# Kernel optimization log

Hardware: AMD Instinct MI355X
Metric: run time of the kernel (lower is better)

Reference implementation:

```python
import jax, jax.numpy as jnp
import numpy as np

DIM_Q = 64
SCALE = DIM_Q ** 0.5


def setup_inputs() -> dict:
    key = jax.random.key(0)
    kq, kk = jax.random.split(key)
    Q = jax.random.normal(kq, (4, 4096, 64), dtype=jnp.float32)
    K = jax.random.normal(kk, (4, 4096, 64), dtype=jnp.float32)
    return {"Q": Q, "K": K}


def _cdist(Q, K):
    # ||q-k||_2 via expansion: ||q||^2 + ||k||^2 - 2 q.k  (matches torch.cdist p=2)
    q2 = jnp.sum(Q * Q, axis=-1, keepdims=True)          # [B,N,1]
    k2 = jnp.sum(K * K, axis=-1)[:, None, :]             # [B,1,M]
    qk = jnp.einsum('bnd,bmd->bnm', Q, K)                # [B,N,M]
    d2 = jnp.maximum(q2 + k2 - 2.0 * qk, 0.0)
    return jnp.sqrt(d2)


def reference(Q, K):
    scores = -_cdist(Q, K) / SCALE                       # [B,N,M]
    return jax.nn.softmax(scores, axis=-1)
```

## Files before the change

kernel.cpp:

```cpp
#include <hip/hip_runtime.h>
#include <hip/hip_bf16.h>

#define BATCH 4
#define NQ 4096
#define NK 4096
#define DIM 64

typedef __attribute__((ext_vector_type(8))) short bf16x8;
typedef __attribute__((ext_vector_type(4))) float f32x4;

__device__ __forceinline__ unsigned short f2bf(float f) {
  union { float f; unsigned u; } v; v.f = f;
  return (unsigned short)((v.u + 0x7FFF + ((v.u >> 16) & 1)) >> 16);
}

template<int ROWS>
__device__ __forceinline__ void stage_tile(const float* __restrict__ g, char* lds,
                                           float* sq, int tid) {
  constexpr int NV = ROWS * 16;
  #pragma unroll
  for (int i = 0; i < NV / 256; ++i) {
    const int idx = i * 256 + tid;
    const float4 v = reinterpret_cast<const float4*>(g)[idx];
    const int f = idx * 4;
    const int row = f >> 6, col = f & 63;
    uint2 pk;
    pk.x = (unsigned)f2bf(v.x) | ((unsigned)f2bf(v.y) << 16);
    pk.y = (unsigned)f2bf(v.z) | ((unsigned)f2bf(v.w) << 16);
    const int byte = row * 128 + ((((col >> 3) ^ (row & 7)) << 4)) + ((col >> 2) & 1) * 8;
    *reinterpret_cast<uint2*>(lds + byte) = pk;
  }
  if (tid < ROWS) {
    const float4* rp = reinterpret_cast<const float4*>(g + tid * DIM);
    float s = 0.f;
    #pragma unroll
    for (int j = 0; j < 16; ++j) {
      const float4 v = rp[j];
      s += v.x * v.x + v.y * v.y + v.z * v.z + v.w * v.w;
    }
    sq[tid] = s;
  }
}

__device__ __forceinline__ bf16x8 frag_load(const char* lds, int row, int ks, int lane) {
  return *reinterpret_cast<const bf16x8*>(
      lds + row * 128 + (((ks * 4 + (lane >> 4)) ^ (row & 7)) << 4));
}

__global__ __launch_bounds__(256) void k_rowsum(
    const float* __restrict__ Qg, const float* __restrict__ Kg,
    float* __restrict__ partials) {
  __shared__ char Qlds[64 * 128];
  __shared__ char Klds[256 * 128];
  __shared__ float q2[64];
  __shared__ float k2[256];
  const int tid = threadIdx.x;
  const int cs = blockIdx.x;
  const int brow = blockIdx.y * 64;
  const int b = blockIdx.z;
  const float* Qb = Qg + ((size_t)b * NQ + brow) * DIM;
  const float* Kb = Kg + (size_t)b * NK * DIM;

  stage_tile<64>(Qb, Qlds, q2, tid);
  __syncthreads();

  const int lane = tid & 63, w = tid >> 6;
  const int arow = w * 16 + (lane & 15);
  const bf16x8 af0 = frag_load(Qlds, arow, 0, lane);
  const bf16x8 af1 = frag_load(Qlds, arow, 1, lane);
  float q2r[4];
  #pragma unroll
  for (int i = 0; i < 4; ++i) q2r[i] = q2[w * 16 + (lane >> 4) * 4 + i];

  float sums[4] = {0.f, 0.f, 0.f, 0.f};
  for (int t = 0; t < 4; ++t) {
    __syncthreads();
    stage_tile<256>(Kb + ((size_t)(cs * 4 + t)) * 256 * DIM, Klds, k2, tid);
    __syncthreads();
    #pragma unroll
    for (int c = 0; c < 16; ++c) {
      const int krow = c * 16 + (lane & 15);
      const bf16x8 bf0 = frag_load(Klds, krow, 0, lane);
      const bf16x8 bf1 = frag_load(Klds, krow, 1, lane);
      f32x4 acc = {0.f, 0.f, 0.f, 0.f};
      acc = __builtin_amdgcn_mfma_f32_16x16x32_bf16(af0, bf0, acc, 0, 0, 0);
      acc = __builtin_amdgcn_mfma_f32_16x16x32_bf16(af1, bf1, acc, 0, 0, 0);
      const float k2c = k2[krow];
      #pragma unroll
      for (int i = 0; i < 4; ++i) {
        const float d2 = fmaxf(q2r[i] + k2c - 2.f * acc[i], 0.f);
        sums[i] += __expf(-sqrtf(d2) * 0.125f);
      }
    }
  }
  #pragma unroll
  for (int m = 1; m < 16; m <<= 1) {
    #pragma unroll
    for (int i = 0; i < 4; ++i) sums[i] += __shfl_xor(sums[i], m, 64);
  }
  if ((lane & 15) == 0) {
    const int r = brow + w * 16 + (lane >> 4) * 4;
    #pragma unroll
    for (int i = 0; i < 4; ++i)
      partials[((size_t)cs * BATCH + b) * NQ + r + i] = sums[i];
  }
}

__global__ __launch_bounds__(256) void k_softmax(
    const float* __restrict__ Qg, const float* __restrict__ Kg,
    const float* __restrict__ partials, float* __restrict__ out) {
  __shared__ char Qlds[64 * 128];
  __shared__ char Klds[256 * 128];
  __shared__ float q2[64];
  __shared__ float k2[256];
  const int tid = threadIdx.x;
  const int bcol = blockIdx.x * 256;
  const int brow = blockIdx.y * 64;
  const int b = blockIdx.z;
  const float* Qb = Qg + ((size_t)b * NQ + brow) * DIM;
  const float* Kb = Kg + ((size_t)b * NK + bcol) * DIM;

  stage_tile<64>(Qb, Qlds, q2, tid);
  stage_tile<256>(Kb, Klds, k2, tid);
  __syncthreads();

  const int lane = tid & 63, w = tid >> 6;
  const int arow = w * 16 + (lane & 15);
  const bf16x8 af0 = frag_load(Qlds, arow, 0, lane);
  const bf16x8 af1 = frag_load(Qlds, arow, 1, lane);

  float q2r[4], inv[4];
  size_t rowbase[4];
  #pragma unroll
  for (int i = 0; i < 4; ++i) {
    const int r = w * 16 + (lane >> 4) * 4 + i;
    q2r[i] = q2[r];
    const int gr = brow + r;
    float s = 0.f;
    #pragma unroll
    for (int cs = 0; cs < 4; ++cs) s += partials[((size_t)cs * BATCH + b) * NQ + gr];
    inv[i] = 1.0f / s;
    rowbase[i] = ((size_t)b * NQ + gr) * NK + bcol;
  }

  #pragma unroll
  for (int c = 0; c < 16; ++c) {
    const int krow = c * 16 + (lane & 15);
    const bf16x8 bf0 = frag_load(Klds, krow, 0, lane);
    const bf16x8 bf1 = frag_load(Klds, krow, 1, lane);
    f32x4 acc = {0.f, 0.f, 0.f, 0.f};
    acc = __builtin_amdgcn_mfma_f32_16x16x32_bf16(af0, bf0, acc, 0, 0, 0);
    acc = __builtin_amdgcn_mfma_f32_16x16x32_bf16(af1, bf1, acc, 0, 0, 0);
    const float k2c = k2[krow];
    const int col = c * 16 + (lane & 15);
    #pragma unroll
    for (int i = 0; i < 4; ++i) {
      const float d2 = fmaxf(q2r[i] + k2c - 2.f * acc[i], 0.f);
      out[rowbase[i] + col] = __expf(-sqrtf(d2) * 0.125f) * inv[i];
    }
  }
}

extern "C" void kernel_launch(void* const* d_in, const int* in_sizes, int n_in,
                              void* d_out, int out_size, void* d_ws, size_t ws_size,
                              hipStream_t stream) {
  const float* Q = (const float*)d_in[0];
  const float* K = (const float*)d_in[1];
  float* out = (float*)d_out;
  float* partials = (float*)d_ws;

  k_rowsum<<<dim3(4, NQ / 64, BATCH), dim3(256), 0, stream>>>(Q, K, partials);
  k_softmax<<<dim3(NK / 256, NQ / 64, BATCH), dim3(256), 0, stream>>>(Q, K, partials, out);
}
```

Baseline: 382.0 us.

## Compute scores once, store fp16 intermediates, then normalize in a separate scaling pass

Replaces the two-pass scheme (row-sum pass then recompute-and-write pass) with a single score pass that writes unnormalized exp values and per-block partial row sums. A small kernel inverts the summed partials and a streaming kernel rescales into the output. The score pass swaps MFMA operands so each lane stores four contiguous columns with vector stores. The fp16 intermediate halves the extra traffic but adds rounding error and needs a large workspace, falling back to in-place fp32 otherwise.

```diff
diff --git a/kernel.cpp b/kernel.cpp
--- a/kernel.cpp
+++ b/kernel.cpp
@@ -1,5 +1,6 @@
 #include <hip/hip_runtime.h>
 #include <hip/hip_bf16.h>
+#include <hip/hip_fp16.h>
 
 #define BATCH 4
 #define NQ 4096
@@ -47,68 +48,10 @@
       lds + row * 128 + (((ks * 4 + (lane >> 4)) ^ (row & 7)) << 4));
 }
 
-__global__ __launch_bounds__(256) void k_rowsum(
+template<bool F16WS>
+__global__ __launch_bounds__(256) void k_score(
     const float* __restrict__ Qg, const float* __restrict__ Kg,
-    float* __restrict__ partials) {
-  __shared__ char Qlds[64 * 128];
-  __shared__ char Klds[256 * 128];
-  __shared__ float q2[64];
-  __shared__ float k2[256];
-  const int tid = threadIdx.x;
-  const int cs = blockIdx.x;
-  const int brow = blockIdx.y * 64;
-  const int b = blockIdx.z;
-  const float* Qb = Qg + ((size_t)b * NQ + brow) * DIM;
-  const float* Kb = Kg + (size_t)b * NK * DIM;
-
-  stage_tile<64>(Qb, Qlds, q2, tid);
-  __syncthreads();
-
-  const int lane = tid & 63, w = tid >> 6;
-  const int arow = w * 16 + (lane & 15);
-  const bf16x8 af0 = frag_load(Qlds, arow, 0, lane);
-  const bf16x8 af1 = frag_load(Qlds, arow, 1, lane);
-  float q2r[4];
-  #pragma unroll
-  for (int i = 0; i < 4; ++i) q2r[i] = q2[w * 16 + (lane >> 4) * 4 + i];
-
-  float sums[4] = {0.f, 0.f, 0.f, 0.f};
-  for (int t = 0; t < 4; ++t) {
-    __syncthreads();
-    stage_tile<256>(Kb + ((size_t)(cs * 4 + t)) * 256 * DIM, Klds, k2, tid);
-    __syncthreads();
-    #pragma unroll
-    for (int c = 0; c < 16; ++c) {
-      const int krow = c * 16 + (lane & 15);
-      const bf16x8 bf0 = frag_load(Klds, krow, 0, lane);
-      const bf16x8 bf1 = frag_load(Klds, krow, 1, lane);
-      f32x4 acc = {0.f, 0.f, 0.f, 0.f};
-      acc = __builtin_amdgcn_mfma_f32_16x16x32_bf16(af0, bf0, acc, 0, 0, 0);
-      acc = __builtin_amdgcn_mfma_f32_16x16x32_bf16(af1, bf1, acc, 0, 0, 0);
-      const float k2c = k2[krow];
-      #pragma unroll
-      for (int i = 0; i < 4; ++i) {
-        const float d2 = fmaxf(q2r[i] + k2c - 2.f * acc[i], 0.f);
-        sums[i] += __expf(-sqrtf(d2) * 0.125f);
-      }
-    }
-  }
-  #pragma unroll
-  for (int m = 1; m < 16; m <<= 1) {
-    #pragma unroll
-    for (int i = 0; i < 4; ++i) sums[i] += __shfl_xor(sums[i], m, 64);
-  }
-  if ((lane & 15) == 0) {
-    const int r = brow + w * 16 + (lane >> 4) * 4;
-    #pragma unroll
-    for (int i = 0; i < 4; ++i)
-      partials[((size_t)cs * BATCH + b) * NQ + r + i] = sums[i];
-  }
-}
-
-__global__ __launch_bounds__(256) void k_softmax(
-    const float* __restrict__ Qg, const float* __restrict__ Kg,
-    const float* __restrict__ partials, float* __restrict__ out) {
+    void* __restrict__ score, float* __restrict__ partials) {
   __shared__ char Qlds[64 * 128];
   __shared__ char Klds[256 * 128];
   __shared__ float q2[64];
@@ -125,39 +68,93 @@
   __syncthreads();
 
   const int lane = tid & 63, w = tid >> 6;
-  const int arow = w * 16 + (lane & 15);
-  const bf16x8 af0 = frag_load(Qlds, arow, 0, lane);
-  const bf16x8 af1 = frag_load(Qlds, arow, 1, lane);
+  const int qrow = w * 16 + (lane & 15);
+  const bf16x8 qf0 = frag_load(Qlds, qrow, 0, lane);
+  const bf16x8 qf1 = frag_load(Qlds, qrow, 1, lane);
+  const float q2r = q2[qrow];
+  const int g = lane >> 4;
 
-  float q2r[4], inv[4];
-  size_t rowbase[4];
-  #pragma unroll
-  for (int i = 0; i < 4; ++i) {
-    const int r = w * 16 + (lane >> 4) * 4 + i;
-    q2r[i] = q2[r];
-    const int gr = brow + r;
-    float s = 0.f;
-    #pragma unroll
-    for (int cs = 0; cs < 4; ++cs) s += partials[((size_t)cs * BATCH + b) * NQ + gr];
-    inv[i] = 1.0f / s;
-    rowbase[i] = ((size_t)b * NQ + gr) * NK + bcol;
-  }
+  float rowsum = 0.f;
+  const size_t rbase = ((size_t)b * NQ + brow + qrow) * NK + bcol + g * 4;
 
   #pragma unroll
   for (int c = 0; c < 16; ++c) {
     const int krow = c * 16 + (lane & 15);
-    const bf16x8 bf0 = frag_load(Klds, krow, 0, lane);
-    const bf16x8 bf1 = frag_load(Klds, krow, 1, lane);
+    const bf16x8 kf0 = frag_load(Klds, krow, 0, lane);
+    const bf16x8 kf1 = frag_load(Klds, krow, 1, lane);
     f32x4 acc = {0.f, 0.f, 0.f, 0.f};
-    acc = __builtin_amdgcn_mfma_f32_16x16x32_bf16(af0, bf0, acc, 0, 0, 0);
-    acc = __builtin_amdgcn_mfma_f32_16x16x32_bf16(af1, bf1, acc, 0, 0, 0);
-    const float k2c = k2[krow];
-    const int col = c * 16 + (lane & 15);
+    acc = __builtin_amdgcn_mfma_f32_16x16x32_bf16(kf0, qf0, acc, 0, 0, 0);
+    acc = __builtin_amdgcn_mfma_f32_16x16x32_bf16(kf1, qf1, acc, 0, 0, 0);
+    const float4 k2v = *reinterpret_cast<const float4*>(k2 + c * 16 + g * 4);
+
+    float e[4];
+    const float k2a[4] = {k2v.x, k2v.y, k2v.z, k2v.w};
     #pragma unroll
     for (int i = 0; i < 4; ++i) {
-      const float d2 = fmaxf(q2r[i] + k2c - 2.f * acc[i], 0.f);
-      out[rowbase[i] + col] = __expf(-sqrtf(d2) * 0.125f) * inv[i];
+      const float d2 = fmaxf(q2r + k2a[i] - 2.f * acc[i], 0.f);
+      e[i] = __expf(-0.125f * sqrtf(d2));
     }
+    if (F16WS) {
+      const __half h0 = __float2half_rn(e[0]), h1 = __float2half_rn(e[1]);
+      const __half h2 = __float2half_rn(e[2]), h3 = __float2half_rn(e[3]);
+      rowsum += __half2float(h0) + __half2float(h1) +
+                __half2float(h2) + __half2float(h3);
+      uint2 pk;
+      pk.x = (unsigned)__half_as_ushort(h0) | ((unsigned)__half_as_ushort(h1) << 16);
+      pk.y = (unsigned)__half_as_ushort(h2) | ((unsigned)__half_as_ushort(h3) << 16);
+      *reinterpret_cast<uint2*>((__half*)score + rbase + c * 16) = pk;
+    } else {
+      rowsum += e[0] + e[1] + e[2] + e[3];
+      float4 st = {e[0], e[1], e[2], e[3]};
+      *reinterpret_cast<float4*>((float*)score + rbase + c * 16) = st;
+    }
+  }
+
+  rowsum += __shfl_xor(rowsum, 16, 64);
+  rowsum += __shfl_xor(rowsum, 32, 64);
+  if (lane < 16)
+    partials[((size_t)blockIdx.x * BATCH + b) * NQ + brow + w * 16 + lane] = rowsum;
+}
+
+__global__ __launch_bounds__(256) void k_inv(
+    const float* __restrict__ partials, float* __restrict__ inv) {
+  const int idx = blockIdx.x * 256 + threadIdx.x;
+  float s = 0.f;
+  #pragma unroll
+  for (int p = 0; p < 16; ++p) s += partials[(size_t)p * (BATCH * NQ) + idx];
+  inv[idx] = 1.f / s;
+}
+
+__global__ __launch_bounds__(256) void k_scale_f16(
+    const __half* __restrict__ sc, const float* __restrict__ inv,
+    float* __restrict__ out) {
+  const size_t nchunk = (size_t)BATCH * NQ * NK / 8;
+  const size_t stride = (size_t)gridDim.x * blockDim.x;
+  for (size_t c = (size_t)blockIdx.x * blockDim.x + threadIdx.x; c < nchunk; c += stride) {
+    const int rg = (int)(c >> 9);
+    const float iv = inv[rg];
+    union { uint4 u; __half h[8]; } U;
+    U.u = reinterpret_cast<const uint4*>(sc)[c];
+    float4 a, bq;
+    a.x = __half2float(U.h[0]) * iv; a.y = __half2float(U.h[1]) * iv;
+    a.z = __half2float(U.h[2]) * iv; a.w = __half2float(U.h[3]) * iv;
+    bq.x = __half2float(U.h[4]) * iv; bq.y = __half2float(U.h[5]) * iv;
+    bq.z = __half2float(U.h[6]) * iv; bq.w = __half2float(U.h[7]) * iv;
+    float4* op = reinterpret_cast<float4*>(out) + 2 * c;
+    op[0] = a; op[1] = bq;
+  }
+}
+
+__global__ __launch_bounds__(256) void k_scale_f32(
+    const float* __restrict__ inv, float* __restrict__ out) {
+  const size_t nchunk = (size_t)BATCH * NQ * NK / 4;
+  const size_t stride = (size_t)gridDim.x * blockDim.x;
+  for (size_t c = (size_t)blockIdx.x * blockDim.x + threadIdx.x; c < nchunk; c += stride) {
+    const int rg = (int)(c >> 10);
+    const float iv = inv[rg];
+    float4 v = reinterpret_cast<float4*>(out)[c];
+    v.x *= iv; v.y *= iv; v.z *= iv; v.w *= iv;
+    reinterpret_cast<float4*>(out)[c] = v;
   }
 }
 
@@ -167,8 +164,23 @@
   const float* Q = (const float*)d_in[0];
   const float* K = (const float*)d_in[1];
   float* out = (float*)d_out;
+
+  const size_t P_BYTES = (size_t)16 * BATCH * NQ * 4;
+  const size_t I_BYTES = (size_t)BATCH * NQ * 4;
+  const size_t S_BYTES = (size_t)BATCH * NQ * NK * 2;
   float* partials = (float*)d_ws;
+  float* inv = (float*)((char*)d_ws + P_BYTES);
+  __half* sc = (__half*)((char*)d_ws + P_BYTES + I_BYTES);
 
-  k_rowsum<<<dim3(4, NQ / 64, BATCH), dim3(256), 0, stream>>>(Q, K, partials);
-  k_softmax<<<dim3(NK / 256, NQ / 64, BATCH), dim3(256), 0, stream>>>(Q, K, partials, out);
+  if (ws_size >= P_BYTES + I_BYTES + S_BYTES) {
+    k_score<true><<<dim3(NK / 256, NQ / 64, BATCH), dim3(256), 0, stream>>>(
+        Q, K, (void*)sc, partials);
+    k_inv<<<dim3(BATCH * NQ / 256), dim3(256), 0, stream>>>(partials, inv);
+    k_scale_f16<<<dim3(2048), dim3(256), 0, stream>>>(sc, inv, out);
+  } else {
+    k_score<false><<<dim3(NK / 256, NQ / 64, BATCH), dim3(256), 0, stream>>>(
+        Q, K, (void*)out, partials);
+    k_inv<<<dim3(BATCH * NQ / 256), dim3(256), 0, stream>>>(partials, inv);
+    k_scale_f32<<<dim3(2048), dim3(256), 0, stream>>>(inv, out);
+  }
 }
```

After: 400.2 us. 1.05x slower.

## Swap MFMA operands so each lane owns a row and stores float4 outputs

Applied to the files above, without the earlier changes.

The MFMA operand order is swapped (K fragment first, Q second), so each lane's four accumulator values fall in one query row across four consecutive key columns. This lets the write kernel emit one 16-byte vectorized store per tile instead of four scattered scalar stores, and lets the row-sum kernel keep a single accumulator reduced with two shuffles. The 1/sum computation moves into a separate small kernel, so the write kernel no longer reads four partials per row. The cost is one extra kernel launch and a small workspace array.

```diff
diff --git a/kernel.cpp b/kernel.cpp
--- a/kernel.cpp
+++ b/kernel.cpp
@@ -65,14 +65,13 @@
   __syncthreads();
 
   const int lane = tid & 63, w = tid >> 6;
-  const int arow = w * 16 + (lane & 15);
-  const bf16x8 af0 = frag_load(Qlds, arow, 0, lane);
-  const bf16x8 af1 = frag_load(Qlds, arow, 1, lane);
-  float q2r[4];
-  #pragma unroll
-  for (int i = 0; i < 4; ++i) q2r[i] = q2[w * 16 + (lane >> 4) * 4 + i];
+  const int qrow = w * 16 + (lane & 15);
+  const bf16x8 qf0 = frag_load(Qlds, qrow, 0, lane);
+  const bf16x8 qf1 = frag_load(Qlds, qrow, 1, lane);
+  const float q2r = q2[qrow];
+  const int g = lane >> 4;
 
-  float sums[4] = {0.f, 0.f, 0.f, 0.f};
+  float rowsum = 0.f;
   for (int t = 0; t < 4; ++t) {
     __syncthreads();
     stage_tile<256>(Kb + ((size_t)(cs * 4 + t)) * 256 * DIM, Klds, k2, tid);
@@ -80,35 +79,38 @@
     #pragma unroll
     for (int c = 0; c < 16; ++c) {
       const int krow = c * 16 + (lane & 15);
-      const bf16x8 bf0 = frag_load(Klds, krow, 0, lane);
-      const bf16x8 bf1 = frag_load(Klds, krow, 1, lane);
+      const bf16x8 kf0 = frag_load(Klds, krow, 0, lane);
+      const bf16x8 kf1 = frag_load(Klds, krow, 1, lane);
       f32x4 acc = {0.f, 0.f, 0.f, 0.f};
-      acc = __builtin_amdgcn_mfma_f32_16x16x32_bf16(af0, bf0, acc, 0, 0, 0);
-      acc = __builtin_amdgcn_mfma_f32_16x16x32_bf16(af1, bf1, acc, 0, 0, 0);
-      const float k2c = k2[krow];
+      acc = __builtin_amdgcn_mfma_f32_16x16x32_bf16(kf0, qf0, acc, 0, 0, 0);
+      acc = __builtin_amdgcn_mfma_f32_16x16x32_bf16(kf1, qf1, acc, 0, 0, 0);
+      const float4 k2v = *reinterpret_cast<const float4*>(k2 + c * 16 + g * 4);
+      const float k2a[4] = {k2v.x, k2v.y, k2v.z, k2v.w};
       #pragma unroll
       for (int i = 0; i < 4; ++i) {
-        const float d2 = fmaxf(q2r[i] + k2c - 2.f * acc[i], 0.f);
-        sums[i] += __expf(-sqrtf(d2) * 0.125f);
+        const float d2 = fmaxf(q2r + k2a[i] - 2.f * acc[i], 0.f);
+        rowsum += __expf(-0.125f * sqrtf(d2));
       }
     }
   }
-  #pragma unroll
-  for (int m = 1; m < 16; m <<= 1) {
-    #pragma unroll
-    for (int i = 0; i < 4; ++i) sums[i] += __shfl_xor(sums[i], m, 64);
-  }
-  if ((lane & 15) == 0) {
-    const int r = brow + w * 16 + (lane >> 4) * 4;
-    #pragma unroll
-    for (int i = 0; i < 4; ++i)
-      partials[((size_t)cs * BATCH + b) * NQ + r + i] = sums[i];
-  }
+  rowsum += __shfl_xor(rowsum, 16, 64);
+  rowsum += __shfl_xor(rowsum, 32, 64);
+  if (lane < 16)
+    partials[((size_t)cs * BATCH + b) * NQ + brow + w * 16 + lane] = rowsum;
 }
 
-__global__ __launch_bounds__(256) void k_softmax(
+__global__ __launch_bounds__(256) void k_inv(
+    const float* __restrict__ partials, float* __restrict__ inv) {
+  const int idx = blockIdx.x * 256 + threadIdx.x;
+  float s = 0.f;
+  #pragma unroll
+  for (int p = 0; p < 4; ++p) s += partials[(size_t)p * (BATCH * NQ) + idx];
+  inv[idx] = 1.f / s;
+}
+
+__global__ __launch_bounds__(256) void k_write(
     const float* __restrict__ Qg, const float* __restrict__ Kg,
-    const float* __restrict__ partials, float* __restrict__ out) {
+    const float* __restrict__ inv, float* __restrict__ out) {
   __shared__ char Qlds[64 * 128];
   __shared__ char Klds[256 * 128];
   __shared__ float q2[64];
@@ -125,39 +127,33 @@
   __syncthreads();
 
   const int lane = tid & 63, w = tid >> 6;
-  const int arow = w * 16 + (lane & 15);
-  const bf16x8 af0 = frag_load(Qlds, arow, 0, lane);
-  const bf16x8 af1 = frag_load(Qlds, arow, 1, lane);
-
-  float q2r[4], inv[4];
-  size_t rowbase[4];
-  #pragma unroll
-  for (int i = 0; i < 4; ++i) {
-    const int r = w * 16 + (lane >> 4) * 4 + i;
-    q2r[i] = q2[r];
-    const int gr = brow + r;
-    float s = 0.f;
-    #pragma unroll
-    for (int cs = 0; cs < 4; ++cs) s += partials[((size_t)cs * BATCH + b) * NQ + gr];
-    inv[i] = 1.0f / s;
-    rowbase[i] = ((size_t)b * NQ + gr) * NK + bcol;
-  }
+  const int qrow = w * 16 + (lane & 15);
+  const bf16x8 qf0 = frag_load(Qlds, qrow, 0, lane);
+  const bf16x8 qf1 = frag_load(Qlds, qrow, 1, lane);
+  const float q2r = q2[qrow];
+  const int g = lane >> 4;
+  const float iv = inv[(size_t)b * NQ + brow + qrow];
+  float* const obase = out + ((size_t)b * NQ + brow + qrow) * NK + bcol + g * 4;
 
   #pragma unroll
   for (int c = 0; c < 16; ++c) {
     const int krow = c * 16 + (lane & 15);
-    const bf16x8 bf0 = frag_load(Klds, krow, 0, lane);
-    const bf16x8 bf1 = frag_load(Klds, krow, 1, lane);
+    const bf16x8 kf0 = frag_load(Klds, krow, 0, lane);
+    const bf16x8 kf1 = frag_load(Klds, krow, 1, lane);
     f32x4 acc = {0.f, 0.f, 0.f, 0.f};
-    acc = __builtin_amdgcn_mfma_f32_16x16x32_bf16(af0, bf0, acc, 0, 0, 0);
-    acc = __builtin_amdgcn_mfma_f32_16x16x32_bf16(af1, bf1, acc, 0, 0, 0);
-    const float k2c = k2[krow];
-    const int col = c * 16 + (lane & 15);
+    acc = __builtin_amdgcn_mfma_f32_16x16x32_bf16(kf0, qf0, acc, 0, 0, 0);
+    acc = __builtin_amdgcn_mfma_f32_16x16x32_bf16(kf1, qf1, acc, 0, 0, 0);
+    const float4 k2v = *reinterpret_cast<const float4*>(k2 + c * 16 + g * 4);
+    const float k2a[4] = {k2v.x, k2v.y, k2v.z, k2v.w};
+    float4 st;
+    float e[4];
     #pragma unroll
     for (int i = 0; i < 4; ++i) {
-      const float d2 = fmaxf(q2r[i] + k2c - 2.f * acc[i], 0.f);
-      out[rowbase[i] + col] = __expf(-sqrtf(d2) * 0.125f) * inv[i];
+      const float d2 = fmaxf(q2r + k2a[i] - 2.f * acc[i], 0.f);
+      e[i] = __expf(-0.125f * sqrtf(d2)) * iv;
     }
+    st.x = e[0]; st.y = e[1]; st.z = e[2]; st.w = e[3];
+    *reinterpret_cast<float4*>(obase + c * 16) = st;
   }
 }
 
@@ -167,8 +163,11 @@
   const float* Q = (const float*)d_in[0];
   const float* K = (const float*)d_in[1];
   float* out = (float*)d_out;
+
   float* partials = (float*)d_ws;
+  float* inv = (float*)((char*)d_ws + (size_t)4 * BATCH * NQ * 4);
 
   k_rowsum<<<dim3(4, NQ / 64, BATCH), dim3(256), 0, stream>>>(Q, K, partials);
-  k_softmax<<<dim3(NK / 256, NQ / 64, BATCH), dim3(256), 0, stream>>>(Q, K, partials, out);
+  k_inv<<<dim3(BATCH * NQ / 256), dim3(256), 0, stream>>>(partials, inv);
+  k_write<<<dim3(NK / 256, NQ / 64, BATCH), dim3(256), 0, stream>>>(Q, K, inv, out);
 }
```

Measured after the change: 369.8 us. 3.2% less time.
